# Kernel optimization log

Hardware: AMD Instinct MI355X
Metric: run time of the kernel (lower is better)

Reference implementation:

```python
import jax, jax.numpy as jnp
import numpy as np
from jax import lax

B, L, T = 16, 128, 1024          # batch, phoneme len, mel frames
D, H, F, NL = 384, 2, 1536, 6    # d_model, heads, ffn dim, layers per stack
V, NMEL, CDP = 128, 80, 256      # vocab, mel bins, duration-predictor channels
NEG = -1e9

def make_posenc(max_pos, d):
    pos = np.arange(max_pos, dtype=np.float32)[:, None]
    i = np.arange(d, dtype=np.float32)[None, :]
    ang = pos / np.power(10000.0, 2.0 * np.floor(i / 2.0) / d)
    pe = np.zeros((max_pos, d), np.float32)
    pe[:, 0::2] = np.sin(ang[:, 0::2])
    pe[:, 1::2] = np.cos(ang[:, 1::2])
    return jnp.asarray(pe)

POS = make_posenc(T, D)

def layer_norm(x, g, b, eps=1e-6):
    m = jnp.mean(x, -1, keepdims=True)
    v = jnp.mean(jnp.square(x - m), -1, keepdims=True)
    return (x - m) * lax.rsqrt(v + eps) * g + b

def mha(x, wq, bq, wk, bk, wv, bv, wo, bo, mask):
    b, s, d = x.shape
    dh = d // H
    def split(t):
        return t.reshape(b, s, H, dh).transpose(0, 2, 1, 3)  # bhsd
    q, k, v = split(x @ wq + bq), split(x @ wk + bk), split(x @ wv + bv)
    logits = jnp.einsum('bhqd,bhkd->bhqk', q, k) / jnp.sqrt(jnp.float32(dh))
    logits = logits + mask * NEG  # mask: [B,1,1,S], 1.0 = masked (as in source)
    w = jax.nn.softmax(logits, axis=-1)
    o = jnp.einsum('bhqk,bhkd->bhqd', w, v).transpose(0, 2, 1, 3).reshape(b, s, d)
    return o @ wo + bo

def fft_stack(x, mask, aw, ab, w1, b1, w2, b2, lnp):
    for i in range(aw.shape[0]):
        a = mha(x, aw[i, 0], ab[i, 0], aw[i, 1], ab[i, 1], aw[i, 2], ab[i, 2], aw[i, 3], ab[i, 3], mask)
        x = layer_norm(x + a, lnp[i, 0, 0], lnp[i, 0, 1])
        f = jax.nn.relu(x @ w1[i] + b1[i]) @ w2[i] + b2[i]
        x = layer_norm(x + f, lnp[i, 1, 0], lnp[i, 1, 1])
    return x

def conv1d_same(x, w, b):
    # x: [B,S,Cin], w: [K,Cin,Cout]
    return lax.conv_general_dilated(x, w, (1,), 'SAME', dimension_numbers=('NWC', 'WIO', 'NWC')) + b

def setup_inputs() -> dict:
    key = jax.random.key(0)
    ks = iter(jax.random.split(key, 24))
    nrm = lambda shape: jax.random.normal(next(ks), shape, jnp.float32) * 0.02
    ln_init = lambda nl, c: jnp.broadcast_to(jnp.stack([jnp.ones(c, jnp.float32), jnp.zeros(c, jnp.float32)]), (nl, 2, 2, c))
    inp = {
        'phonemes': jax.random.randint(next(ks), (B, L), 1, V, jnp.int32),
        'durations': jax.random.randint(next(ks), (B, L), 1, 16, jnp.int32),
        'embed': nrm((V, D)),
        'alpha_enc': jnp.float32(1.0),
        'alpha_dec': jnp.float32(1.0),
        'enc_attn_w': nrm((NL, 4, D, D)), 'enc_attn_b': jnp.zeros((NL, 4, D), jnp.float32),
        'enc_ffn_w1': nrm((NL, D, F)), 'enc_ffn_b1': jnp.zeros((NL, F), jnp.float32),
        'enc_ffn_w2': nrm((NL, F, D)), 'enc_ffn_b2': jnp.zeros((NL, D), jnp.float32),
        'enc_ln': ln_init(NL, D),
        'dec_attn_w': nrm((NL, 4, D, D)), 'dec_attn_b': jnp.zeros((NL, 4, D), jnp.float32),
        'dec_ffn_w1': nrm((NL, D, F)), 'dec_ffn_b1': jnp.zeros((NL, F), jnp.float32),
        'dec_ffn_w2': nrm((NL, F, D)), 'dec_ffn_b2': jnp.zeros((NL, D), jnp.float32),
        'dec_ln': ln_init(NL, D),
        'dp_conv1_w': nrm((3, D, CDP)), 'dp_conv1_b': jnp.zeros((CDP,), jnp.float32),
        'dp_conv2_w': nrm((3, CDP, CDP)), 'dp_conv2_b': jnp.zeros((CDP,), jnp.float32),
        'dp_ln': jnp.broadcast_to(jnp.stack([jnp.ones(CDP, jnp.float32), jnp.zeros(CDP, jnp.float32)]), (2, 2, CDP)),
        'dp_out_w': nrm((CDP, 1)), 'dp_out_b': jnp.zeros((1,), jnp.float32),
        'mel_w': nrm((D, NMEL)), 'mel_b': jnp.zeros((NMEL,), jnp.float32),
    }
    return inp

def reference(phonemes, durations, embed, alpha_enc, alpha_dec,
              enc_attn_w, enc_attn_b, enc_ffn_w1, enc_ffn_b1, enc_ffn_w2, enc_ffn_b2, enc_ln,
              dec_attn_w, dec_attn_b, dec_ffn_w1, dec_ffn_b1, dec_ffn_w2, dec_ffn_b2, dec_ln,
              dp_conv1_w, dp_conv1_b, dp_conv2_w, dp_conv2_b, dp_ln, dp_out_w, dp_out_b,
              mel_w, mel_b):
    Lp = phonemes.shape[1]
    # phoneme encoder with scaled positional encoding
    x = embed[phonemes] + alpha_enc * POS[None, :Lp, :]
    enc_mask = (phonemes == 0).astype(jnp.float32)[:, None, None, :]
    h = fft_stack(x, enc_mask, enc_attn_w, enc_attn_b, enc_ffn_w1, enc_ffn_b1, enc_ffn_w2, enc_ffn_b2, enc_ln)
    # duration predictor: conv1d -> relu -> LN, x2, then linear (log durations)
    d1 = layer_norm(jax.nn.relu(conv1d_same(h, dp_conv1_w, dp_conv1_b)), dp_ln[0, 0], dp_ln[0, 1])
    d2 = layer_norm(jax.nn.relu(conv1d_same(d1, dp_conv2_w, dp_conv2_b)), dp_ln[1, 0], dp_ln[1, 1])
    dur_pred = (d2 @ dp_out_w + dp_out_b)[..., 0]  # [B, L]
    # length regulator: expand each phoneme state by its (teacher) duration via gather
    cum = jnp.cumsum(durations, axis=1)  # [B, L]
    frames = jnp.arange(T)
    idx = jax.vmap(lambda c: jnp.searchsorted(c, frames, side='right'))(cum)  # [B, T]
    idx = jnp.clip(idx, 0, Lp - 1)
    y = jnp.take_along_axis(h, idx[:, :, None], axis=1)  # [B, T, D]
    valid = (frames[None, :] < cum[:, -1:]).astype(jnp.float32)  # [B, T]
    y = y * valid[:, :, None]
    # mel decoder
    y = y + alpha_dec * POS[None, :T, :]
    dec_mask = (1.0 - valid)[:, None, None, :]
    m = fft_stack(y, dec_mask, dec_attn_w, dec_attn_b, dec_ffn_w1, dec_ffn_b1, dec_ffn_w2, dec_ffn_b2, dec_ln)
    mel = m @ mel_w + mel_b  # [B, T, NMEL]
    return mel, dur_pred
```

## Files before the change

kernel.cpp:

```cpp
#include <hip/hip_runtime.h>
#include <math.h>

#define BATCH 16
#define LPH 128
#define TFR 1024
#define DMODEL 384
#define FDIM 1536
#define NLAYER 6
#define NMELB 80
#define CDPC 256
#define NEGV (-1e9f)

typedef unsigned short u16;
typedef __attribute__((ext_vector_type(8))) short short8;
typedef __attribute__((ext_vector_type(4))) float f32x4;

__device__ __forceinline__ float b2f(u16 u) {
  return __uint_as_float(((unsigned)u) << 16);
}
__device__ __forceinline__ u16 f2b(float f) {
  unsigned x = __float_as_uint(f);
  return (u16)((x + 0x7fffu + ((x >> 16) & 1u)) >> 16);
}
__device__ __forceinline__ unsigned cvtpk(float lo, float hi) {
  unsigned r;
  asm volatile("v_cvt_pk_bf16_f32 %0, %1, %2" : "=v"(r) : "v"(lo), "v"(hi));
  return r;
}

#define GLOAD16(gp, lp)                                                                   \
  __builtin_amdgcn_global_load_lds((const __attribute__((address_space(1))) void*)(gp),   \
                                   (__attribute__((address_space(3))) void*)(lp), 16, 0, 0)

#define FBIAS 1
#define FRES 2
#define FRELU 4
#define FOB16 8
#define FVT 16

#define GSW(r, c) ((r) * 64 + ((c) ^ (((r)&7) << 3)))
template <int FL>
__global__ __launch_bounds__(256) void bgemm(
    const u16* __restrict__ A, const u16* __restrict__ Bt,
    const float* __restrict__ bias, const float* __restrict__ res,
    void* __restrict__ Cv, u16* __restrict__ VtP,
    int N, int K, int lda, int ldb, int ldc,
    int zdiv, long az0, long az1, long bz0, long bz1, long cz0, long cz1, int S) {
  constexpr int SMEMSZ = (FL & FVT) ? (128 * 136) : 16384;
  __shared__ __align__(16) u16 smem[SMEMSZ];
  u16* As = smem;
  u16* Bs = smem + 8192;
  const int tid = threadIdx.x;
  const int wave = tid >> 6, lane = tid & 63;
  const int wm = wave >> 1, wn = wave & 1;
  const int lrow = lane & 15, lk = lane >> 4;
  const int z = blockIdx.z;
  const int zq = z / zdiv, zr = z - zq * zdiv;
  const long offA = (long)zq * az0 + (long)zr * az1;
  const long offB = (long)zq * bz0 + (long)zr * bz1;
  const long offC = (long)zq * cz0 + (long)zr * cz1;
  const int fid = blockIdx.x + gridDim.x * blockIdx.y;
  const int idx = fid >> 3;
  const int xl = idx % gridDim.x;
  const int yl = (fid & 7) + 8 * (idx / gridDim.x);
  const int row0 = yl * 128;
  const int col0 = xl * 128;

  const u16* gA[4];
  const u16* gB[4];
  u16* lA[4];
  u16* lB[4];
#pragma unroll
  for (int i = 0; i < 4; i++) {
    int c = tid + i * 256;
    int r = c >> 3, cg = c & 7;
    int swz = ((cg ^ (r & 7)) * 8);
    gA[i] = A + offA + (long)(row0 + r) * lda + swz;
    gB[i] = Bt + offB + (long)(col0 + r) * ldb + swz;
    lA[i] = As + c * 8;
    lB[i] = Bs + c * 8;
  }

  f32x4 acc[4][4];
  const f32x4 zero4 = {0.f, 0.f, 0.f, 0.f};
#pragma unroll
  for (int i = 0; i < 4; i++)
#pragma unroll
    for (int j = 0; j < 4; j++) acc[i][j] = zero4;

  for (int k0 = 0; k0 < K; k0 += 64) {
#pragma unroll
    for (int i = 0; i < 4; i++) {
      GLOAD16(gA[i], lA[i]);
      GLOAD16(gB[i], lB[i]);
    }
#pragma unroll
    for (int i = 0; i < 4; i++) { gA[i] += 64; gB[i] += 64; }
    __syncthreads();
#pragma unroll
    for (int kk = 0; kk < 2; kk++) {
      short8 av[4], bv[4];
#pragma unroll
      for (int mi = 0; mi < 4; mi++)
        av[mi] = *(const short8*)&As[GSW(wm * 64 + mi * 16 + lrow, kk * 32 + lk * 8)];
#pragma unroll
      for (int ni = 0; ni < 4; ni++)
        bv[ni] = *(const short8*)&Bs[GSW(wn * 64 + ni * 16 + lrow, kk * 32 + lk * 8)];
#pragma unroll
      for (int mi = 0; mi < 4; mi++)
#pragma unroll
        for (int ni = 0; ni < 4; ni++)
          acc[mi][ni] = __builtin_amdgcn_mfma_f32_16x16x32_bf16(av[mi], bv[ni], acc[mi][ni], 0, 0, 0);
    }
    __syncthreads();
  }

  const float* bz = (FL & FBIAS) ? bias + (long)z * N : nullptr;
  if constexpr ((FL & FVT) != 0) {
    if (z == 2) {
      u16* Ts = smem;
#pragma unroll
      for (int mi = 0; mi < 4; mi++) {
        int si = wm * 64 + lk * 4 + mi * 16;
#pragma unroll
        for (int ni = 0; ni < 4; ni++) {
          int cl = wn * 64 + ni * 16 + lrow;
          float bi = bz[col0 + cl];
          uint2 oo;
          oo.x = cvtpk(acc[mi][ni][0] + bi, acc[mi][ni][1] + bi);
          oo.y = cvtpk(acc[mi][ni][2] + bi, acc[mi][ni][3] + bi);
          *(uint2*)&Ts[cl * 136 + si] = oo;
        }
      }
      __syncthreads();
      const int ci = tid >> 1;
      const int cbase = (tid & 1) * 64;
      int c = col0 + ci;
      int hh = c / 192, dd = c - hh * 192;
      int bb = row0 / S;
      int ss = row0 % S;
      u16* dst = &VtP[((long)(bb * 2 + hh) * 256 + dd) * S + ss + cbase];
      const u16* srcr = &Ts[ci * 136 + cbase];
#pragma unroll
      for (int j = 0; j < 8; j++)
        *(short8*)&dst[j * 8] = *(const short8*)&srcr[j * 8];
      return;
    }
  }
  float* Cf = (float*)Cv + offC;
  u16* Cb = (u16*)Cv + offC;
  const float* resz = (FL & FRES) ? res + offC : nullptr;
#pragma unroll
  for (int mi = 0; mi < 4; mi++) {
    long rbase = row0 + wm * 64 + lk * 4 + (long)mi * 16;
#pragma unroll
    for (int ni = 0; ni < 4; ni++) {
      int c = col0 + wn * 64 + ni * 16 + lrow;
      if (c < N) {
        float bi = (FL & FBIAS) ? bz[c] : 0.f;
#pragma unroll
        for (int rr = 0; rr < 4; rr++) {
          float vv = acc[mi][ni][rr] + bi;
          if (FL & FRES) vv += resz[(rbase + rr) * (long)ldc + c];
          if (FL & FRELU) vv = fmaxf(vv, 0.f);
          if (FL & FOB16) Cb[(rbase + rr) * (long)ldc + c] = f2b(vv);
          else Cf[(rbase + rr) * (long)ldc + c] = vv;
        }
      }
    }
  }
}

#define KSW(r, c) ((r) * 192 + ((c) ^ (((r)&7) << 3)))
#define VSTR 72
#define PSTR 72
__global__ __launch_bounds__(512) void fattn(const u16* __restrict__ qb,
                                             const u16* __restrict__ kb,
                                             const u16* __restrict__ vt,
                                             const float* __restrict__ maska,
                                             u16* __restrict__ opart,
                                             float* __restrict__ mlpart,
                                             int S, int qtshift) {
  __shared__ __align__(16) u16 Ks[64 * 192];
  __shared__ __align__(16) u16 Vs[192 * VSTR];
  __shared__ __align__(16) u16 PsT[8][16 * PSTR];
  const int tid = threadIdx.x;
  const int w = tid >> 6, l = tid & 63;
  const int g = l >> 4, lr = l & 15;
  const int QT = gridDim.x;
  const int fid = (blockIdx.z * 32 + blockIdx.y) * QT + blockIdx.x;
  const int s = fid >> 3;
  const int gid = (fid & 7) * 8 + (s >> qtshift);
  const int qt = s & (QT - 1);
  const int bh = gid & 31, z = gid >> 5;
  const int b = bh >> 1, h = bh & 1;
  const int q0 = qt * 128 + w * 16;
  const int hoff = h * 192;
  const int KS = S >> 1;
  const int kbeg = z * KS;
  const float scale = 0.0721687836f;

  int kr[3], kc[3], vr[3], vc[3];
#pragma unroll
  for (int i = 0; i < 3; i++) {
    int c = tid + i * 512;
    kr[i] = c / 24; kc[i] = (c % 24) * 8;
    vr[i] = c >> 3; vc[i] = (c & 7) * 8;
  }
  const u16* kbase = kb + (long)b * S * 384 + hoff;
  const u16* vbase = vt + (long)bh * 256 * S;

  const long qrowb = ((long)b * S + q0 + lr) * 384 + hoff + g * 8;
  short8 qf[6];
#pragma unroll
  for (int ks = 0; ks < 6; ks++) qf[ks] = *(const short8*)&qb[qrowb + ks * 32];

  f32x4 accO[12];
  const f32x4 zero4 = {0.f, 0.f, 0.f, 0.f};
#pragma unroll
  for (int j = 0; j < 12; j++) accO[j] = zero4;
  float m = -1e30f, lsum = 0.f;

  short8 kst[3], vst[3];
#pragma unroll
  for (int i = 0; i < 3; i++) {
    kst[i] = *(const short8*)&kbase[(long)(kbeg + kr[i]) * 384 + kc[i]];
    vst[i] = *(const short8*)&vbase[(long)vr[i] * S + kbeg + vc[i]];
  }

  for (int kt = kbeg; kt < kbeg + KS; kt += 64) {
    __syncthreads();
#pragma unroll
    for (int i = 0; i < 3; i++) {
      *(short8*)&Ks[KSW(kr[i], kc[i])] = kst[i];
      *(short8*)&Vs[vr[i] * VSTR + vc[i]] = vst[i];
    }
    __syncthreads();
    if (kt + 64 < kbeg + KS) {
#pragma unroll
      for (int i = 0; i < 3; i++) {
        kst[i] = *(const short8*)&kbase[(long)(kt + 64 + kr[i]) * 384 + kc[i]];
        vst[i] = *(const short8*)&vbase[(long)vr[i] * S + kt + 64 + vc[i]];
      }
    }
    f32x4 sacc[4];
#pragma unroll
    for (int f = 0; f < 4; f++) sacc[f] = zero4;
    __builtin_amdgcn_s_setprio(1);
#pragma unroll
    for (int ks = 0; ks < 6; ks++) {
#pragma unroll
      for (int f = 0; f < 4; f++) {
        short8 kf = *(const short8*)&Ks[KSW(f * 16 + lr, ks * 32 + g * 8)];
        sacc[f] = __builtin_amdgcn_mfma_f32_16x16x32_bf16(kf, qf[ks], sacc[f], 0, 0, 0);
      }
    }
    __builtin_amdgcn_s_setprio(0);
#pragma unroll
    for (int f = 0; f < 4; f++) {
      if (maska) {
        float4 mk4 = *(const float4*)&maska[(long)b * S + kt + f * 16 + 4 * g];
        sacc[f][0] = fmaf(sacc[f][0], scale, mk4.x);
        sacc[f][1] = fmaf(sacc[f][1], scale, mk4.y);
        sacc[f][2] = fmaf(sacc[f][2], scale, mk4.z);
        sacc[f][3] = fmaf(sacc[f][3], scale, mk4.w);
      } else {
#pragma unroll
        for (int r = 0; r < 4; r++) sacc[f][r] *= scale;
      }
    }
    float tm = sacc[0][0];
#pragma unroll
    for (int f = 0; f < 4; f++)
#pragma unroll
      for (int r = 0; r < 4; r++) tm = fmaxf(tm, sacc[f][r]);
    tm = fmaxf(tm, __shfl_xor(tm, 16));
    tm = fmaxf(tm, __shfl_xor(tm, 32));
    if (__any(tm > m + 8.f)) {
      float mn = fmaxf(m, tm);
      float al = __expf(m - mn);
      m = mn;
      lsum *= al;
#pragma unroll
      for (int j = 0; j < 12; j++)
#pragma unroll
        for (int r = 0; r < 4; r++) accO[j][r] *= al;
    }
    float rs = 0.f;
#pragma unroll
    for (int f = 0; f < 4; f++)
#pragma unroll
      for (int r = 0; r < 4; r++) {
        float p = __expf(sacc[f][r] - m);
        sacc[f][r] = p;
        rs += p;
      }
    rs += __shfl_xor(rs, 16);
    rs += __shfl_xor(rs, 32);
    lsum += rs;
#pragma unroll
    for (int f = 0; f < 4; f++) {
      uint2 pp;
      pp.x = cvtpk(sacc[f][0], sacc[f][1]);
      pp.y = cvtpk(sacc[f][2], sacc[f][3]);
      *(uint2*)&PsT[w][lr * PSTR + f * 16 + 4 * g] = pp;
    }
    __builtin_amdgcn_s_setprio(1);
#pragma unroll
    for (int ks = 0; ks < 2; ks++) {
      short8 pT = *(const short8*)&PsT[w][lr * PSTR + ks * 32 + g * 8];
#pragma unroll
      for (int j = 0; j < 12; j++) {
        short8 vf = *(const short8*)&Vs[(j * 16 + lr) * VSTR + ks * 32 + g * 8];
        accO[j] = __builtin_amdgcn_mfma_f32_16x16x32_bf16(vf, pT, accO[j], 0, 0, 0);
      }
    }
    __builtin_amdgcn_s_setprio(0);
  }
  const long orow = ((long)(z * 32 + bh) * S + q0 + lr) * 192;
#pragma unroll
  for (int j = 0; j < 12; j++) {
    uint2 oo;
    oo.x = cvtpk(accO[j][0], accO[j][1]);
    oo.y = cvtpk(accO[j][2], accO[j][3]);
    *(uint2*)&opart[orow + j * 16 + 4 * g] = oo;
  }
  if (g == 0) {
    long mi = ((long)(z * 32 + bh) * S + q0 + lr) * 2;
    mlpart[mi] = m;
    mlpart[mi + 1] = lsum;
  }
}

__global__ __launch_bounds__(256) void fmerge(const u16* __restrict__ opart,
                                              const float* __restrict__ mlpart,
                                              u16* __restrict__ ob, int S) {
  long cid = (long)blockIdx.x * 256 + threadIdx.x;
  long nch = (long)32 * S * 24;
  if (cid >= nch) return;
  int row = (int)(cid / 24);
  int c8 = (int)(cid % 24) * 8;
  int bh = row / S, q = row - bh * S;
  int b = bh >> 1, h = bh & 1;
  long zs = (long)32 * S;
  float m0 = mlpart[(long)row * 2], l0 = mlpart[(long)row * 2 + 1];
  float m1 = mlpart[(zs + row) * 2], l1 = mlpart[(zs + row) * 2 + 1];
  float M = fmaxf(m0, m1);
  float a0 = __expf(m0 - M), a1 = __expf(m1 - M);
  float invL = 1.f / (a0 * l0 + a1 * l1);
  a0 *= invL; a1 *= invL;
  short8 o0 = *(const short8*)&opart[(long)row * 192 + c8];
  short8 o1 = *(const short8*)&opart[zs * 192 + (long)row * 192 + c8];
  float v[8];
#pragma unroll
  for (int j = 0; j < 8; j++)
    v[j] = a0 * b2f((u16)o0[j]) + a1 * b2f((u16)o1[j]);
  uint4 oo;
  oo.x = cvtpk(v[0], v[1]);
  oo.y = cvtpk(v[2], v[3]);
  oo.z = cvtpk(v[4], v[5]);
  oo.w = cvtpk(v[6], v[7]);
  *(uint4*)&ob[((long)b * S + q) * 384 + h * 192 + c8] = oo;
}

__global__ void wconv_t(const float* __restrict__ src, u16* __restrict__ dst, int K, int N) {
  __shared__ float t[32][33];
  long mb = blockIdx.z;
  src += mb * (long)K * N;
  dst += mb * (long)K * N;
  int n0 = blockIdx.x * 32, k0 = blockIdx.y * 32;
  int tx = threadIdx.x, ty = threadIdx.y;
#pragma unroll
  for (int i = 0; i < 4; i++) {
    int r = ty + i * 8;
    t[r][tx] = src[(long)(k0 + r) * N + n0 + tx];
  }
  __syncthreads();
#pragma unroll
  for (int i = 0; i < 4; i++) {
    int r = ty + i * 8;
    dst[(long)(n0 + r) * K + k0 + tx] = f2b(t[tx][r]);
  }
}

__global__ void melw_t(const float* __restrict__ src, u16* __restrict__ dst) {
  int i = blockIdx.x * 256 + threadIdx.x;
  if (i >= 128 * 384) return;
  int n = i / 384, kk2 = i - n * 384;
  dst[i] = (n < NMELB) ? f2b(src[(long)kk2 * NMELB + n]) : (u16)0;
}

__global__ void posenc_kernel(float* __restrict__ pe) {
  int i = blockIdx.x * 256 + threadIdx.x;
  if (i >= TFR * DMODEL) return;
  int t = i / DMODEL, d = i - t * DMODEL;
  float f = (2.0f * (float)(d >> 1)) / (float)DMODEL;
  float ang = (float)t * powf(10000.0f, -f);
  pe[i] = (d & 1) ? cosf(ang) : sinf(ang);
}

__global__ void embed_kernel(const int* __restrict__ ph, const float* __restrict__ emb,
                             const float* __restrict__ pe, const float* __restrict__ alpha,
                             u16* __restrict__ xb) {
  int i = blockIdx.x * 256 + threadIdx.x;
  if (i >= BATCH * LPH * DMODEL) return;
  int d = i % DMODEL;
  int bl = i / DMODEL;
  int l = bl % LPH;
  float v = emb[ph[bl] * DMODEL + d] + alpha[0] * pe[l * DMODEL + d];
  xb[i] = f2b(v);
}

template <int C>
__global__ __launch_bounds__(256) void lnw(float* __restrict__ x, const float* __restrict__ gamma,
                                           const float* __restrict__ beta,
                                           float* __restrict__ outf, u16* __restrict__ outb) {
  const int w = threadIdx.x >> 6, l = threadIdx.x & 63;
  const long row = (long)blockIdx.x * 4 + w;
  constexpr int NL = C / 8;
  float* xr = x + row * C;
  float v[8];
  float s1 = 0.f, s2 = 0.f;
  if (l < NL) {
    float4 a = *(const float4*)&xr[8 * l];
    float4 bq = *(const float4*)&xr[8 * l + 4];
    v[0] = a.x; v[1] = a.y; v[2] = a.z; v[3] = a.w;
    v[4] = bq.x; v[5] = bq.y; v[6] = bq.z; v[7] = bq.w;
#pragma unroll
    for (int j = 0; j < 8; j++) { s1 += v[j]; s2 += v[j] * v[j]; }
  }
#pragma unroll
  for (int off = 1; off < 64; off <<= 1) {
    s1 += __shfl_xor(s1, off);
    s2 += __shfl_xor(s2, off);
  }
  float mean = s1 / C;
  float var = s2 / C - mean * mean;
  float rstd = rsqrtf(var + 1e-6f);
  if (l < NL) {
    float4 g0 = *(const float4*)&gamma[8 * l];
    float4 g1 = *(const float4*)&gamma[8 * l + 4];
    float4 b0 = *(const float4*)&beta[8 * l];
    float4 b1 = *(const float4*)&beta[8 * l + 4];
    float o[8];
    o[0] = (v[0] - mean) * rstd * g0.x + b0.x;
    o[1] = (v[1] - mean) * rstd * g0.y + b0.y;
    o[2] = (v[2] - mean) * rstd * g0.z + b0.z;
    o[3] = (v[3] - mean) * rstd * g0.w + b0.w;
    o[4] = (v[4] - mean) * rstd * g1.x + b1.x;
    o[5] = (v[5] - mean) * rstd * g1.y + b1.y;
    o[6] = (v[6] - mean) * rstd * g1.z + b1.z;
    o[7] = (v[7] - mean) * rstd * g1.w + b1.w;
    float* tf = outf ? outf + row * C : xr;
    *(float4*)&tf[8 * l] = make_float4(o[0], o[1], o[2], o[3]);
    *(float4*)&tf[8 * l + 4] = make_float4(o[4], o[5], o[6], o[7]);
    if (outb) {
      uint4 ob4;
      ob4.x = cvtpk(o[0], o[1]);
      ob4.y = cvtpk(o[2], o[3]);
      ob4.z = cvtpk(o[4], o[5]);
      ob4.w = cvtpk(o[6], o[7]);
      *(uint4*)&outb[row * C + 8 * l] = ob4;
    }
  }
}

template <int C>
__global__ __launch_bounds__(256) void lnsum(const u16* __restrict__ p0, const u16* __restrict__ p1,
                                             const float* __restrict__ bias,
                                             const u16* __restrict__ resb,
                                             const float* __restrict__ gamma,
                                             const float* __restrict__ beta,
                                             float* __restrict__ outf, u16* __restrict__ outb) {
  const int w = threadIdx.x >> 6, l = threadIdx.x & 63;
  const long row = (long)blockIdx.x * 4 + w;
  constexpr int NL = C / 8;
  float v[8];
  float s1 = 0.f, s2 = 0.f;
  if (l < NL) {
    short8 a = *(const short8*)&p0[row * C + 8 * l];
    short8 bq = *(const short8*)&p1[row * C + 8 * l];
    short8 r = *(const short8*)&resb[row * C + 8 * l];
    float4 bi0 = *(const float4*)&bias[8 * l];
    float4 bi1 = *(const float4*)&bias[8 * l + 4];
    const float* bip = &bi0.x;
#pragma unroll
    for (int j = 0; j < 8; j++) {
      float bb = (j < 4) ? (&bi0.x)[j] : (&bi1.x)[j - 4];
      v[j] = b2f((u16)a[j]) + b2f((u16)bq[j]) + bb + b2f((u16)r[j]);
      s1 += v[j];
      s2 += v[j] * v[j];
    }
    (void)bip;
  }
#pragma unroll
  for (int off = 1; off < 64; off <<= 1) {
    s1 += __shfl_xor(s1, off);
    s2 += __shfl_xor(s2, off);
  }
  float mean = s1 / C;
  float var = s2 / C - mean * mean;
  float rstd = rsqrtf(var + 1e-6f);
  if (l < NL) {
    float4 g0 = *(const float4*)&gamma[8 * l];
    float4 g1 = *(const float4*)&gamma[8 * l + 4];
    float4 b0 = *(const float4*)&beta[8 * l];
    float4 b1 = *(const float4*)&beta[8 * l + 4];
    float o[8];
    o[0] = (v[0] - mean) * rstd * g0.x + b0.x;
    o[1] = (v[1] - mean) * rstd * g0.y + b0.y;
    o[2] = (v[2] - mean) * rstd * g0.z + b0.z;
    o[3] = (v[3] - mean) * rstd * g0.w + b0.w;
    o[4] = (v[4] - mean) * rstd * g1.x + b1.x;
    o[5] = (v[5] - mean) * rstd * g1.y + b1.y;
    o[6] = (v[6] - mean) * rstd * g1.z + b1.z;
    o[7] = (v[7] - mean) * rstd * g1.w + b1.w;
    if (outf) {
      *(float4*)&outf[row * C + 8 * l] = make_float4(o[0], o[1], o[2], o[3]);
      *(float4*)&outf[row * C + 8 * l + 4] = make_float4(o[4], o[5], o[6], o[7]);
    }
    if (outb) {
      uint4 ob4;
      ob4.x = cvtpk(o[0], o[1]);
      ob4.y = cvtpk(o[2], o[3]);
      ob4.z = cvtpk(o[4], o[5]);
      ob4.w = cvtpk(o[6], o[7]);
      *(uint4*)&outb[row * C + 8 * l] = ob4;
    }
  }
}

template <int CIN>
__global__ __launch_bounds__(256) void im2col3(const float* __restrict__ x,
                                               u16* __restrict__ a) {
  const int PER = (3 * CIN) / 8;
  long idx = (long)blockIdx.x * 256 + threadIdx.x;
  if (idx >= (long)BATCH * LPH * PER) return;
  int row = (int)(idx / PER);
  int e8 = (int)(idx - (long)row * PER) * 8;
  int kk = e8 / CIN, ci = e8 - kk * CIN;
  int b = row >> 7, l = row & (LPH - 1);
  int gl = l + kk - 1;
  ushort4 o0 = {0, 0, 0, 0}, o1 = {0, 0, 0, 0};
  if (gl >= 0 && gl < LPH) {
    const float* src = x + ((long)(b * LPH + gl) * CIN + ci);
    float4 v0 = *(const float4*)src;
    float4 v1 = *(const float4*)(src + 4);
    o0.x = f2b(v0.x); o0.y = f2b(v0.y); o0.z = f2b(v0.z); o0.w = f2b(v0.w);
    o1.x = f2b(v1.x); o1.y = f2b(v1.y); o1.z = f2b(v1.z); o1.w = f2b(v1.w);
  }
  *(ushort4*)&a[(long)row * (3 * CIN) + e8] = o0;
  *(ushort4*)&a[(long)row * (3 * CIN) + e8 + 4] = o1;
}

__global__ void dpout_kernel(const float* __restrict__ d2, const float* __restrict__ w,
                             const float* __restrict__ bb, float* __restrict__ out) {
  int wv = threadIdx.x >> 6, lane = threadIdx.x & 63;
  int row = blockIdx.x * 4 + wv;
  const float* xr = d2 + (long)row * CDPC;
  float s = 0.f;
  for (int c = lane; c < CDPC; c += 64) s = fmaf(xr[c], w[c], s);
#pragma unroll
  for (int off = 32; off > 0; off >>= 1) s += __shfl_down(s, off);
  if (lane == 0) out[row] = s + bb[0];
}

__global__ void regulator_kernel(const int* __restrict__ durations, int* __restrict__ idx,
                                 float* __restrict__ maskv, float* __restrict__ maska) {
  __shared__ int cum[LPH];
  __shared__ int total;
  int b = blockIdx.x;
  if (threadIdx.x == 0) {
    int s = 0;
    for (int j = 0; j < LPH; j++) { s += durations[b * LPH + j]; cum[j] = s; }
    total = s;
  }
  __syncthreads();
  for (int t = threadIdx.x; t < TFR; t += blockDim.x) {
    int cnt = 0;
    for (int j = 0; j < LPH; j++) cnt += (cum[j] <= t) ? 1 : 0;
    if (cnt > LPH - 1) cnt = LPH - 1;
    idx[b * TFR + t] = cnt;
    maskv[b * TFR + t] = (t < total) ? 0.f : 1.f;
    maska[b * TFR + t] = (t < total) ? 0.f : NEGV;
  }
}

__global__ void gather_kernel(const float* __restrict__ h, const int* __restrict__ idx,
                              const float* __restrict__ maskv, const float* __restrict__ pe,
                              const float* __restrict__ alpha, u16* __restrict__ yb) {
  long i = (long)blockIdx.x * 256 + threadIdx.x;
  if (i >= (long)BATCH * TFR * DMODEL) return;
  int d = (int)(i % DMODEL);
  long bt = i / DMODEL;
  int t = (int)(bt % TFR);
  long b = bt / TFR;
  float valid = 1.0f - maskv[bt];
  float v = h[((long)b * LPH + idx[bt]) * DMODEL + d] * valid + alpha[0] * pe[t * DMODEL + d];
  yb[i] = f2b(v);
}

extern "C" void kernel_launch(void* const* d_in, const int* in_sizes, int n_in,
                              void* d_out, int out_size, void* d_ws, size_t ws_size,
                              hipStream_t stream) {
  const int* phonemes = (const int*)d_in[0];
  const int* durations = (const int*)d_in[1];
  const float* embedw = (const float*)d_in[2];
  const float* alpha_enc = (const float*)d_in[3];
  const float* alpha_dec = (const float*)d_in[4];
  const float* enc_attn_w = (const float*)d_in[5];
  const float* enc_attn_b = (const float*)d_in[6];
  const float* enc_ffn_w1 = (const float*)d_in[7];
  const float* enc_ffn_b1 = (const float*)d_in[8];
  const float* enc_ffn_w2 = (const float*)d_in[9];
  const float* enc_ffn_b2 = (const float*)d_in[10];
  const float* enc_ln = (const float*)d_in[11];
  const float* dec_attn_w = (const float*)d_in[12];
  const float* dec_attn_b = (const float*)d_in[13];
  const float* dec_ffn_w1 = (const float*)d_in[14];
  const float* dec_ffn_b1 = (const float*)d_in[15];
  const float* dec_ffn_w2 = (const float*)d_in[16];
  const float* dec_ffn_b2 = (const float*)d_in[17];
  const float* dec_ln = (const float*)d_in[18];
  const float* dp_conv1_w = (const float*)d_in[19];
  const float* dp_conv1_b = (const float*)d_in[20];
  const float* dp_conv2_w = (const float*)d_in[21];
  const float* dp_conv2_b = (const float*)d_in[22];
  const float* dp_ln = (const float*)d_in[23];
  const float* dp_out_w = (const float*)d_in[24];
  const float* dp_out_b = (const float*)d_in[25];
  const float* mel_w = (const float*)d_in[26];
  const float* mel_b = (const float*)d_in[27];

  char* base = (char*)d_ws;
  u16* FP = (u16*)base;
  u16* Xb = (u16*)(base + 25165824);
  u16* QKb = (u16*)(base + 37748736);
  char* E = base + 62914560;
  u16* Vt = (u16*)(base + 96468992);
  u16* Wb = (u16*)(base + 113246208);
  float* Henc = (float*)(base + 134479872);
  float* PE = (float*)(base + 137625600);
  float* MASKD = (float*)(base + 139198464);
  int* IDX = (int*)(base + 139264000);
  u16* Wmel = (u16*)(base + 139329536);
  float* MASKA = (float*)(base + 139427840);

  u16* AOb = QKb;
  u16* Mb = QKb;

  u16* OPART = (u16*)E;
  float* MLPART = (float*)(E + 25165824);
  u16* AOP = (u16*)E;

  float* DP1 = (float*)E;
  float* DP2 = DP1 + (size_t)2048 * CDPC;
  u16* A1 = (u16*)(E + 4 * 1024 * 1024);
  u16* A2 = (u16*)(E + 9 * 1024 * 1024);
  u16* Wdp1 = (u16*)(E + 13 * 1024 * 1024);
  u16* Wdp2 = (u16*)(E + 15 * 1024 * 1024);

  u16* WAt = Wb;
  u16* W1t = Wb + 3538944;
  u16* W2t = Wb + 7077888;

  const int Me = BATCH * LPH;
  const int Md = BATCH * TFR;
  const long DD = 384L * 384;
  const long NXe = (long)Me * DMODEL;
  const long NXd = (long)Md * DMODEL;
  dim3 tb32(32, 8);

  posenc_kernel<<<(TFR * DMODEL + 255) / 256, 256, 0, stream>>>(PE);
  embed_kernel<<<(Me * DMODEL + 255) / 256, 256, 0, stream>>>(phonemes, embedw, PE, alpha_enc, Xb);
  wconv_t<<<dim3(12, 12, 24), tb32, 0, stream>>>(enc_attn_w, WAt, 384, 384);
  wconv_t<<<dim3(48, 12, 6), tb32, 0, stream>>>(enc_ffn_w1, W1t, 384, 1536);
  wconv_t<<<dim3(12, 48, 6), tb32, 0, stream>>>(enc_ffn_w2, W2t, 1536, 384);
  melw_t<<<192, 256, 0, stream>>>(mel_w, Wmel);

  for (int i = 0; i < NLAYER; i++) {
    const u16* wa = WAt + (size_t)i * 4 * DD;
    const float* ab = enc_attn_b + (size_t)i * 4 * 384;
    bgemm<(FBIAS | FOB16 | FVT)><<<dim3(3, 16, 3), 256, 0, stream>>>(
        Xb, wa, ab, nullptr, QKb, Vt, 384, 384, 384, 384, 384,
        1, 0, 0, DD, 0, NXe, 0, 128);
    fattn<<<dim3(1, 32, 2), 512, 0, stream>>>(QKb, QKb + NXe, Vt, nullptr, OPART, MLPART, 128, 0);
    fmerge<<<384, 256, 0, stream>>>(OPART, MLPART, AOb, 128);
    bgemm<(FOB16)><<<dim3(3, 16, 2), 256, 0, stream>>>(
        AOb, wa + 3 * DD, nullptr, nullptr, AOP, nullptr, 384, 192, 384, 384, 384,
        2, 0, 192, 0, 192, 0, NXe, 0);
    lnsum<384><<<Me / 4, 256, 0, stream>>>(AOP, AOP + NXe, ab + 3 * 384, Xb,
                                           enc_ln + ((size_t)(i * 2 + 0) * 2 + 0) * 384,
                                           enc_ln + ((size_t)(i * 2 + 0) * 2 + 1) * 384,
                                           nullptr, Xb);
    bgemm<(FBIAS | FRELU | FOB16)><<<dim3(12, 16, 1), 256, 0, stream>>>(
        Xb, W1t + (size_t)i * 589824, enc_ffn_b1 + (size_t)i * 1536, nullptr, Mb, nullptr,
        1536, 384, 384, 384, 1536, 1, 0, 0, 0, 0, 0, 0, 0);
    bgemm<(FOB16)><<<dim3(3, 16, 2), 256, 0, stream>>>(
        Mb, W2t + (size_t)i * 589824, nullptr, nullptr, FP, nullptr,
        384, 768, 1536, 1536, 384, 2, 0, 768, 0, 768, 0, NXe, 0);
    lnsum<384><<<Me / 4, 256, 0, stream>>>(FP, FP + NXe, enc_ffn_b2 + (size_t)i * 384, Xb,
                                           enc_ln + ((size_t)(i * 2 + 1) * 2 + 0) * 384,
                                           enc_ln + ((size_t)(i * 2 + 1) * 2 + 1) * 384,
                                           (i == NLAYER - 1) ? Henc : nullptr, Xb);
  }

  wconv_t<<<dim3(8, 36, 1), tb32, 0, stream>>>(dp_conv1_w, Wdp1, 1152, 256);
  wconv_t<<<dim3(8, 24, 1), tb32, 0, stream>>>(dp_conv2_w, Wdp2, 768, 256);
  im2col3<DMODEL><<<(Me * 144 + 255) / 256, 256, 0, stream>>>(Henc, A1);
  bgemm<(FBIAS | FRELU)><<<dim3(2, 16, 1), 256, 0, stream>>>(
      A1, Wdp1, dp_conv1_b, nullptr, DP1, nullptr, 256, 1152, 1152, 1152, 256,
      1, 0, 0, 0, 0, 0, 0, 0);
  lnw<256><<<Me / 4, 256, 0, stream>>>(DP1, dp_ln + 0 * CDPC, dp_ln + 1 * CDPC, nullptr, nullptr);
  im2col3<CDPC><<<(Me * 96 + 255) / 256, 256, 0, stream>>>(DP1, A2);
  bgemm<(FBIAS | FRELU)><<<dim3(2, 16, 1), 256, 0, stream>>>(
      A2, Wdp2, dp_conv2_b, nullptr, DP2, nullptr, 256, 768, 768, 768, 256,
      1, 0, 0, 0, 0, 0, 0, 0);
  lnw<256><<<Me / 4, 256, 0, stream>>>(DP2, dp_ln + 2 * CDPC, dp_ln + 3 * CDPC, nullptr, nullptr);
  float* durout = (float*)d_out + (size_t)Md * NMELB;
  dpout_kernel<<<Me / 4, 256, 0, stream>>>(DP2, dp_out_w, dp_out_b, durout);

  regulator_kernel<<<BATCH, 256, 0, stream>>>(durations, IDX, MASKD, MASKA);
  gather_kernel<<<(int)((NXd + 255) / 256), 256, 0, stream>>>(Henc, IDX, MASKD, PE, alpha_dec, Xb);
  wconv_t<<<dim3(12, 12, 24), tb32, 0, stream>>>(dec_attn_w, WAt, 384, 384);
  wconv_t<<<dim3(48, 12, 6), tb32, 0, stream>>>(dec_ffn_w1, W1t, 384, 1536);
  wconv_t<<<dim3(12, 48, 6), tb32, 0, stream>>>(dec_ffn_w2, W2t, 1536, 384);

  for (int i = 0; i < NLAYER; i++) {
    const u16* wa = WAt + (size_t)i * 4 * DD;
    const float* ab = dec_attn_b + (size_t)i * 4 * 384;
    bgemm<(FBIAS | FOB16 | FVT)><<<dim3(3, 128, 3), 256, 0, stream>>>(
        Xb, wa, ab, nullptr, QKb, Vt, 384, 384, 384, 384, 384,
        1, 0, 0, DD, 0, NXd, 0, 1024);
    fattn<<<dim3(8, 32, 2), 512, 0, stream>>>(QKb, QKb + NXd, Vt, MASKA, OPART, MLPART, 1024, 3);
    fmerge<<<3072, 256, 0, stream>>>(OPART, MLPART, AOb, 1024);
    bgemm<(FOB16)><<<dim3(3, 128, 2), 256, 0, stream>>>(
        AOb, wa + 3 * DD, nullptr, nullptr, AOP, nullptr, 384, 192, 384, 384, 384,
        2, 0, 192, 0, 192, 0, NXd, 0);
    lnsum<384><<<Md / 4, 256, 0, stream>>>(AOP, AOP + NXd, ab + 3 * 384, Xb,
                                           dec_ln + ((size_t)(i * 2 + 0) * 2 + 0) * 384,
                                           dec_ln + ((size_t)(i * 2 + 0) * 2 + 1) * 384,
                                           nullptr, Xb);
    bgemm<(FBIAS | FRELU | FOB16)><<<dim3(12, 128, 1), 256, 0, stream>>>(
        Xb, W1t + (size_t)i * 589824, dec_ffn_b1 + (size_t)i * 1536, nullptr, Mb, nullptr,
        1536, 384, 384, 384, 1536, 1, 0, 0, 0, 0, 0, 0, 0);
    bgemm<(FOB16)><<<dim3(3, 128, 2), 256, 0, stream>>>(
        Mb, W2t + (size_t)i * 589824, nullptr, nullptr, FP, nullptr,
        384, 768, 1536, 1536, 384, 2, 0, 768, 0, 768, 0, NXd, 0);
    lnsum<384><<<Md / 4, 256, 0, stream>>>(FP, FP + NXd, dec_ffn_b2 + (size_t)i * 384, Xb,
                                           dec_ln + ((size_t)(i * 2 + 1) * 2 + 0) * 384,
                                           dec_ln + ((size_t)(i * 2 + 1) * 2 + 1) * 384,
                                           nullptr, Xb);
  }

  bgemm<(FBIAS)><<<dim3(1, 128, 1), 256, 0, stream>>>(
      Xb, Wmel, mel_b, nullptr, (float*)d_out, nullptr, 80, 384, 384, 384, 80,
      1, 0, 0, 0, 0, 0, 0, 0);
}
```

Baseline: 1.671 ms.

## Double-buffer GEMM LDS tiles with K=32 steps and a new swizzle

The bf16 GEMM main loop now uses two 4096-element LDS buffers per operand with a K-step of 32. It prefetches the next tile via global_load_lds while MFMAs run on the current one, replacing the load, sync, compute pattern over 64-wide K tiles. The LDS layout changes to pack two rows per 64-element line with a new XOR swizzle. The change trades one sync per 64 K for one per 32 K and relies on the compiler not stalling on vmcnt before the reads of the current buffer.

New measurement: 1.676 ms. No clear change (+0.3%).

```diff
diff --git a/kernel.cpp b/kernel.cpp
--- a/kernel.cpp
+++ b/kernel.cpp
@@ -38,7 +38,7 @@
 #define FOB16 8
 #define FVT 16
 
-#define GSW(r, c) ((r) * 64 + ((c) ^ (((r)&7) << 3)))
+#define DSW(p, hl) ((p) * 64 + ((hl) ^ ((p)&7)) * 8)
 template <int FL>
 __global__ __launch_bounds__(256) void bgemm(
     const u16* __restrict__ A, const u16* __restrict__ Bt,
@@ -48,8 +48,6 @@
     int zdiv, long az0, long az1, long bz0, long bz1, long cz0, long cz1, int S) {
   constexpr int SMEMSZ = (FL & FVT) ? (128 * 136) : 16384;
   __shared__ __align__(16) u16 smem[SMEMSZ];
-  u16* As = smem;
-  u16* Bs = smem + 8192;
   const int tid = threadIdx.x;
   const int wave = tid >> 6, lane = tid & 63;
   const int wm = wave >> 1, wn = wave & 1;
@@ -66,19 +64,17 @@
   const int row0 = yl * 128;
   const int col0 = xl * 128;
 
-  const u16* gA[4];
-  const u16* gB[4];
-  u16* lA[4];
-  u16* lB[4];
-#pragma unroll
-  for (int i = 0; i < 4; i++) {
+  const u16* gA[2];
+  const u16* gB[2];
+  int lofs[2];
+#pragma unroll
+  for (int i = 0; i < 2; i++) {
     int c = tid + i * 256;
-    int r = c >> 3, cg = c & 7;
-    int swz = ((cg ^ (r & 7)) * 8);
-    gA[i] = A + offA + (long)(row0 + r) * lda + swz;
-    gB[i] = Bt + offB + (long)(col0 + r) * ldb + swz;
-    lA[i] = As + c * 8;
-    lB[i] = Bs + c * 8;
+    int p = c >> 3, s = c & 7, u = s ^ (p & 7);
+    int grow = 2 * p + (u >> 2), gcol = (u & 3) * 8;
+    gA[i] = A + offA + (long)(row0 + grow) * lda + gcol;
+    gB[i] = Bt + offB + (long)(col0 + grow) * ldb + gcol;
+    lofs[i] = c * 8;
   }
 
   f32x4 acc[4][4];
@@ -88,31 +84,45 @@
 #pragma unroll
     for (int j = 0; j < 4; j++) acc[i][j] = zero4;
 
-  for (int k0 = 0; k0 < K; k0 += 64) {
-#pragma unroll
-    for (int i = 0; i < 4; i++) {
-      GLOAD16(gA[i], lA[i]);
-      GLOAD16(gB[i], lB[i]);
-    }
-#pragma unroll
-    for (int i = 0; i < 4; i++) { gA[i] += 64; gB[i] += 64; }
+#pragma unroll
+  for (int i = 0; i < 2; i++) {
+    GLOAD16(gA[i], smem + lofs[i]);
+    GLOAD16(gB[i], smem + 8192 + lofs[i]);
+  }
+#pragma unroll
+  for (int i = 0; i < 2; i++) { gA[i] += 32; gB[i] += 32; }
+  __syncthreads();
+
+  const int nt = K >> 5;
+  int cur = 0;
+  for (int t = 0; t < nt; t++) {
+    if (t + 1 < nt) {
+#pragma unroll
+      for (int i = 0; i < 2; i++) {
+        GLOAD16(gA[i], smem + (cur ^ 1) * 4096 + lofs[i]);
+        GLOAD16(gB[i], smem + 8192 + (cur ^ 1) * 4096 + lofs[i]);
+      }
+#pragma unroll
+      for (int i = 0; i < 2; i++) { gA[i] += 32; gB[i] += 32; }
+    }
+    short8 av[4], bv[4];
+#pragma unroll
+    for (int mi = 0; mi < 4; mi++) {
+      int arow = wm * 64 + mi * 16 + lrow;
+      av[mi] = *(const short8*)&smem[cur * 4096 + DSW(arow >> 1, ((arow & 1) << 2) | lk)];
+    }
+#pragma unroll
+    for (int ni = 0; ni < 4; ni++) {
+      int brow = wn * 64 + ni * 16 + lrow;
+      bv[ni] = *(const short8*)&smem[8192 + cur * 4096 + DSW(brow >> 1, ((brow & 1) << 2) | lk)];
+    }
+#pragma unroll
+    for (int mi = 0; mi < 4; mi++)
+#pragma unroll
+      for (int ni = 0; ni < 4; ni++)
+        acc[mi][ni] = __builtin_amdgcn_mfma_f32_16x16x32_bf16(av[mi], bv[ni], acc[mi][ni], 0, 0, 0);
     __syncthreads();
-#pragma unroll
-    for (int kk = 0; kk < 2; kk++) {
-      short8 av[4], bv[4];
-#pragma unroll
-      for (int mi = 0; mi < 4; mi++)
-        av[mi] = *(const short8*)&As[GSW(wm * 64 + mi * 16 + lrow, kk * 32 + lk * 8)];
-#pragma unroll
-      for (int ni = 0; ni < 4; ni++)
-        bv[ni] = *(const short8*)&Bs[GSW(wn * 64 + ni * 16 + lrow, kk * 32 + lk * 8)];
-#pragma unroll
-      for (int mi = 0; mi < 4; mi++)
-#pragma unroll
-        for (int ni = 0; ni < 4; ni++)
-          acc[mi][ni] = __builtin_amdgcn_mfma_f32_16x16x32_bf16(av[mi], bv[ni], acc[mi][ni], 0, 0, 0);
-    }
-    __syncthreads();
+    cur ^= 1;
   }
 
   const float* bz = (FL & FBIAS) ? bias + (long)z * N : nullptr;
@@ -483,7 +493,6 @@
     short8 r = *(const short8*)&resb[row * C + 8 * l];
     float4 bi0 = *(const float4*)&bias[8 * l];
     float4 bi1 = *(const float4*)&bias[8 * l + 4];
-    const float* bip = &bi0.x;
 #pragma unroll
     for (int j = 0; j < 8; j++) {
       float bb = (j < 4) ? (&bi0.x)[j] : (&bi1.x)[j - 4];
@@ -491,7 +500,6 @@
       s1 += v[j];
       s2 += v[j] * v[j];
     }
-    (void)bip;
   }
 #pragma unroll
   for (int off = 1; off < 64; off <<= 1) {
```
